# Performance work log

Measured on AMD Instinct MI355X. Metric: run time of the kernel, lower is better.

The kernel has to match this reference:

```python
import jax, jax.numpy as jnp
import numpy as np
from jax import lax

H = 512          # m_rnn_units
DIL = 2          # dilation
FH = 96          # forecast_horizon


def gru_step(x, h, Wih, Whh, bih, bhh):
    # torch.nn.GRU cell math
    gi = x @ Wih.T + bih          # [N, 3H]
    gh = h @ Whh.T + bhh          # [N, 3H]
    i_r, i_z, i_n = jnp.split(gi, 3, axis=-1)
    h_r, h_z, h_n = jnp.split(gh, 3, axis=-1)
    r = jax.nn.sigmoid(i_r + h_r)
    z = jax.nn.sigmoid(i_z + h_z)
    n = jnp.tanh(i_n + r * h_n)
    return (1.0 - z) * n + z * h


def setup_inputs() -> dict:
    key = jax.random.key(0)
    ks = jax.random.split(key, 10)
    s = 0.05
    return {
        "X0": jax.random.normal(ks[0], (64, 2 * H, 512), dtype=jnp.float32),
        "X1": jax.random.normal(ks[1], (64, H, FH), dtype=jnp.float32),
        "seqlen": 512,
        "W_ih_enc": jax.random.normal(ks[2], (3 * H, 2 * H), dtype=jnp.float32) * s,
        "W_hh_enc": jax.random.normal(ks[3], (3 * H, H), dtype=jnp.float32) * s,
        "b_ih_enc": jax.random.normal(ks[4], (3 * H,), dtype=jnp.float32) * s,
        "b_hh_enc": jax.random.normal(ks[5], (3 * H,), dtype=jnp.float32) * s,
        "W_ih_dec": jax.random.normal(ks[6], (3 * H, 2 * H), dtype=jnp.float32) * s,
        "W_hh_dec": jax.random.normal(ks[7], (3 * H, H), dtype=jnp.float32) * s,
        "b_ih_dec": jax.random.normal(ks[8], (3 * H,), dtype=jnp.float32) * s,
        "b_hh_dec": jax.random.normal(ks[9], (3 * H,), dtype=jnp.float32) * s,
    }


def reference(X0, X1, seqlen, W_ih_enc, W_hh_enc, b_ih_enc, b_hh_enc,
              W_ih_dec, W_hh_dec, b_ih_dec, b_hh_dec):
    B, C, T = X0.shape
    tgt_len = FH // DIL + 1
    N = B * DIL

    # ---- dilation reshuffle of history ----
    T2 = DIL * (T // DIL)
    X0c = X0[:, :, T - T2:]
    XX0 = jnp.stack([X0c[:, :, i::DIL] for i in range(DIL)])   # [d, B, C, T/d]
    XX0 = XX0.reshape(N, C, -1).transpose(0, 2, 1)             # [N, T/d, C]

    # ---- encoder GRU (scan over time) ----
    h0 = jnp.zeros((N, H), X0.dtype)

    def enc_step(h, xt):
        h2 = gru_step(xt, h, W_ih_enc, W_hh_enc, b_ih_enc, b_hh_enc)
        return h2, None

    h_enc, _ = lax.scan(enc_step, h0, XX0.transpose(1, 0, 2))  # [N, H]

    # ---- dilation reshuffle of covariates, pad to tgt_len*DIL ----
    pad = tgt_len * DIL - X1.shape[-1]
    X1p = jnp.pad(X1, ((0, 0), (0, 0), (0, pad)))
    XX1 = jnp.stack([X1p[:, :, i::DIL] for i in range(DIL)]).reshape(N, H, tgt_len)
    xs = XX1.transpose(2, 0, 1)                                # [tgt_len, N, H]

    def dec_step(carry, x1t):
        h, din = carry
        x = jnp.concatenate([din, x1t], axis=-1)               # [N, 2H]
        h2 = gru_step(x, h, W_ih_dec, W_hh_dec, b_ih_dec, b_hh_dec)
        return (h2, h2), h2

    _, outs = lax.scan(dec_step, (h_enc, h_enc), xs)           # [tgt_len, N, H]

    # ---- de-interleave back to original time order ----
    o = outs.transpose(1, 2, 0)                                # [N, H, tgt_len]
    o = o.reshape(DIL, B, H, tgt_len).transpose(1, 2, 3, 0)    # [B, H, tgt_len, d]
    o = o.reshape(B, H, tgt_len * DIL)
    return o[:, :, :FH]
```

## Files before the change

kernel.cpp:

```cpp
#include <hip/hip_runtime.h>


typedef __bf16 bf16x8 __attribute__((ext_vector_type(8)));
typedef float  f32x4  __attribute__((ext_vector_type(4)));
typedef unsigned int u32x4 __attribute__((ext_vector_type(4)));

#define MFMA16(a, b, c) __builtin_amdgcn_mfma_f32_16x16x32_bf16(a, b, c, 0, 0, 0)

#define OFF_FLG   0ULL
#define OFF_HB    16384ULL
#define OFF_XX0H  540672ULL
#define OFF_XX0L  67649536ULL
#define OFF_XX1H  134758400ULL
#define OFF_XX1L  141049856ULL
#define NEED_FULL 147341312ULL

static __device__ __forceinline__ void split_bf(float x, unsigned short& hi,
                                                unsigned short& lo) {
  union { __bf16 b; unsigned short u; } c;
  c.b = (__bf16)x; hi = c.u;
  float fh = (float)c.b;
  c.b = (__bf16)(x - fh); lo = c.u;
}
static __device__ __forceinline__ void split8(const float* __restrict__ p,
                                              bf16x8& h, bf16x8& l) {
#pragma unroll
  for (int j = 0; j < 8; ++j) {
    const float x = p[j];
    const __bf16 hb = (__bf16)x;
    h[j] = hb;
    l[j] = (__bf16)(x - (float)hb);
  }
}
static __device__ __forceinline__ void split8a(const float* xv, bf16x8& h, bf16x8& l) {
#pragma unroll
  for (int j = 0; j < 8; ++j) {
    const float x = xv[j];
    const __bf16 hb = (__bf16)x;
    h[j] = hb;
    l[j] = (__bf16)(x - (float)hb);
  }
}
static __device__ __forceinline__ float sigmoidf_(float x) {
  return 1.0f / (1.0f + __expf(-x));
}
static __device__ __forceinline__ float tanhf_(float x) {
  x = fminf(fmaxf(x, -15.0f), 15.0f);
  float e = __expf(2.0f * x);
  return (e - 1.0f) / (e + 1.0f);
}

static __device__ __forceinline__ void store_u32_mall(unsigned int* p,
                                                      unsigned int v) {
  asm volatile("global_store_dword %0, %1, off sc0 sc1"
               :: "v"(p), "v"(v) : "memory");
}
static __device__ __forceinline__ unsigned int load_u32_mall(const unsigned int* p) {
  unsigned int v;
  asm volatile("global_load_dword %0, %1, off sc0 sc1\n\t"
               "s_waitcnt vmcnt(0)"
               : "=v"(v) : "v"(p) : "memory");
  return v;
}
static __device__ __forceinline__ void load_h8_mall(const unsigned int* base,
                                                    u32x4 hv[4][2]) {
  asm volatile(
      "global_load_dwordx4 %0, %8, off sc0 sc1\n\t"
      "global_load_dwordx4 %1, %8, off offset:16 sc0 sc1\n\t"
      "global_load_dwordx4 %2, %8, off offset:128 sc0 sc1\n\t"
      "global_load_dwordx4 %3, %8, off offset:144 sc0 sc1\n\t"
      "global_load_dwordx4 %4, %8, off offset:256 sc0 sc1\n\t"
      "global_load_dwordx4 %5, %8, off offset:272 sc0 sc1\n\t"
      "global_load_dwordx4 %6, %8, off offset:384 sc0 sc1\n\t"
      "global_load_dwordx4 %7, %8, off offset:400 sc0 sc1\n\t"
      "s_waitcnt vmcnt(0)"
      : "=&v"(hv[0][0]), "=&v"(hv[0][1]), "=&v"(hv[1][0]), "=&v"(hv[1][1]),
        "=&v"(hv[2][0]), "=&v"(hv[2][1]), "=&v"(hv[3][0]), "=&v"(hv[3][1])
      : "v"(base)
      : "memory");
}

static __device__ __forceinline__ void wait_group(const unsigned int* __restrict__ flg,
                                                  int wave, int lane, unsigned int tgt) {
  if (wave == 0) {
    const unsigned int* fp = flg + (size_t)lane * 16;
    for (unsigned int it = 0; it < (1u << 20); ++it) {
      unsigned int v = tgt;
      if (lane < 32) v = load_u32_mall(fp);
      if (__all((int)(v >= tgt))) break;
      __builtin_amdgcn_s_sleep(1);
    }
  }
  __syncthreads();
}

static __device__ __forceinline__ void publish_group(unsigned int* myfl, int tid,
                                                     unsigned int val) {
  asm volatile("s_waitcnt vmcnt(0)" ::: "memory");
  __syncthreads();
  if (tid == 0) store_u32_mall(myfl, val);
}

__global__ void prep_x0(const float* __restrict__ X0, unsigned short* __restrict__ XH) {
  unsigned short* XL = XH + 33554432;
  __shared__ float tile[32][65];
  const int b  = blockIdx.x;
  const int c0 = blockIdx.y * 32;
  const int tid = threadIdx.x;
  for (int tb = 0; tb < 8; ++tb) {
    const int tau0 = tb * 64;
#pragma unroll
    for (int i = 0; i < 8; ++i) {
      const int cc  = (tid >> 6) + 4 * i;
      const int tau = tid & 63;
      tile[cc][tau] = X0[(size_t)b * 524288 + (size_t)(c0 + cc) * 512 + tau0 + tau];
    }
    __syncthreads();
#pragma unroll
    for (int s = 0; s < 8; ++s) {
      const int cc  = tid & 31;
      const int tau = (tid >> 5) * 8 + s;
      const int gt  = tau0 + tau;
      const int tt  = gt >> 1, d = gt & 1;
      unsigned short h, l;
      split_bf(tile[cc][tau], h, l);
      const size_t o = (size_t)tt * 131072 + (size_t)(d * 64 + b) * 1024 + c0 + cc;
      XH[o] = h; XL[o] = l;
    }
    __syncthreads();
  }
}

__global__ void prep_x1(const float* __restrict__ X1, unsigned short* __restrict__ XH) {
  unsigned short* XL = XH + 3145728;
  __shared__ float tile[32][97];
  const int b  = blockIdx.x;
  const int h0 = blockIdx.y * 32;
  const int tid = threadIdx.x;
#pragma unroll
  for (int i = 0; i < 12; ++i) {
    const int idx = i * 256 + tid;
    const int cc = idx / 96, tau = idx % 96;
    tile[cc][tau] = X1[(size_t)b * 49152 + (size_t)(h0 + cc) * 96 + tau];
  }
  __syncthreads();
#pragma unroll
  for (int i = 0; i < 12; ++i) {
    const int idx = i * 256 + tid;
    const int cc = idx & 31, tau = idx >> 5;
    const int tt = tau >> 1, d = tau & 1;
    unsigned short h, l;
    split_bf(tile[cc][tau], h, l);
    const size_t o = (size_t)tt * 65536 + (size_t)(d * 64 + b) * 512 + h0 + cc;
    XH[o] = h; XL[o] = l;
  }
}

template <bool STAGED>
__launch_bounds__(256, 1)
__global__ void rnn_persistent(unsigned char* __restrict__ ws,
                               const float* __restrict__ X0, const float* __restrict__ X1,
                               const float* __restrict__ WihE, const float* __restrict__ WhhE,
                               const float* __restrict__ bihE, const float* __restrict__ bhhE,
                               const float* __restrict__ WihD, const float* __restrict__ WhhD,
                               const float* __restrict__ bihD, const float* __restrict__ bhhD,
                               float* __restrict__ out) {
  const int tid  = threadIdx.x;
  const int wave = tid >> 6;
  const int lane = tid & 63;
  const int l15  = lane & 15;
  const int quad = lane >> 4;

  const int g  = blockIdx.x & 7;
  const int m  = blockIdx.x >> 3;
  const int rb = g * 16;
  const int ib = m * 16;

  const unsigned short* XX0H = (const unsigned short*)(ws + OFF_XX0H);
  const unsigned short* XX0L = (const unsigned short*)(ws + OFF_XX0L);
  const unsigned short* XX1H = (const unsigned short*)(ws + OFF_XX1H);
  const unsigned short* XX1L = (const unsigned short*)(ws + OFF_XX1L);
  unsigned int* HbP  = (unsigned int*)(ws + OFF_HB);
  unsigned int* flg  = (unsigned int*)(ws + OFF_FLG) + (size_t)g * 512;
  unsigned int* myfl = flg + (size_t)m * 16;

  __shared__ float red[4][6][256];

  const int r_row = tid >> 4;
  const int ii    = tid & 15;
  const int ig    = ib + ii;

  const int an    = rb + l15;
  const int ab    = an & 63, ad = an >> 6;
  const int onrow = rb + r_row;
  const int ob    = onrow & 63, od = onrow >> 6;

  const float bieR = bihE[ig], bieZ = bihE[512 + ig], bieN = bihE[1024 + ig];
  const float bheR = bhhE[ig], bheZ = bhhE[512 + ig], bheN = bhhE[1024 + ig];
  const float bidR = bihD[ig], bidZ = bihD[512 + ig], bidN = bihD[1024 + ig];
  const float bhdR = bhhD[ig], bhdZ = bhhD[512 + ig], bhdN = bhhD[1024 + ig];

  bf16x8 WIH_H[24], WIH_L[24], WHH_H[12], WHH_L[12];
#pragma unroll
  for (int kt = 0; kt < 8; ++kt)
#pragma unroll
    for (int nt = 0; nt < 3; ++nt)
      split8(WihE + (size_t)(nt * 512 + ib + l15) * 1024 + (wave * 8 + kt) * 32 + quad * 8,
             WIH_H[kt * 3 + nt], WIH_L[kt * 3 + nt]);
#pragma unroll
  for (int kt = 0; kt < 4; ++kt)
#pragma unroll
    for (int nt = 0; nt < 3; ++nt)
      split8(WhhE + (size_t)(nt * 512 + ib + l15) * 512 + (wave * 4 + kt) * 32 + quad * 8,
             WHH_H[kt * 3 + nt], WHH_L[kt * 3 + nt]);

  float h_reg = 0.0f;
  store_u32_mall(HbP + (size_t)onrow * 512 + ig, 0u);
  publish_group(myfl, tid, 1u);

  for (int t = 0; t < 256; ++t) {
    const int par  = t & 1;
    const int wpar = (t + 1) & 1;

    f32x4 gi0 = {0,0,0,0}, gi1 = {0,0,0,0}, gi2 = {0,0,0,0};
    const size_t xb  = ((size_t)t * 128 + an) * 1024 + quad * 8;
    const int    tau = 2 * t + ad;
#pragma unroll
    for (int kt = 0; kt < 8; ++kt) {
      bf16x8 axh, axl;
      if constexpr (STAGED) {
        axh = *reinterpret_cast<const bf16x8*>(XX0H + xb + (wave * 8 + kt) * 32);
        axl = *reinterpret_cast<const bf16x8*>(XX0L + xb + (wave * 8 + kt) * 32);
      } else {
        float xv[8];
#pragma unroll
        for (int j = 0; j < 8; ++j)
          xv[j] = X0[(size_t)ab * 524288 +
                     (size_t)((wave * 8 + kt) * 32 + quad * 8 + j) * 512 + tau];
        split8a(xv, axh, axl);
      }
      gi0 = MFMA16(axh, WIH_H[kt * 3 + 0], gi0);
      gi1 = MFMA16(axh, WIH_H[kt * 3 + 1], gi1);
      gi2 = MFMA16(axh, WIH_H[kt * 3 + 2], gi2);
      gi0 = MFMA16(axl, WIH_H[kt * 3 + 0], gi0);
      gi1 = MFMA16(axl, WIH_H[kt * 3 + 1], gi1);
      gi2 = MFMA16(axl, WIH_H[kt * 3 + 2], gi2);
      gi0 = MFMA16(axh, WIH_L[kt * 3 + 0], gi0);
      gi1 = MFMA16(axh, WIH_L[kt * 3 + 1], gi1);
      gi2 = MFMA16(axh, WIH_L[kt * 3 + 2], gi2);
    }

    wait_group(flg, wave, lane, (unsigned int)(t + 1));

    const unsigned int* hrow = HbP + (size_t)par * 65536 + (size_t)an * 512 + quad * 8;
    u32x4 hv[4][2];
    load_h8_mall(hrow + (size_t)wave * 128, hv);
    __builtin_amdgcn_sched_barrier(0);

    f32x4 gh0 = {0,0,0,0}, gh1 = {0,0,0,0}, gh2 = {0,0,0,0};
#pragma unroll
    for (int kt = 0; kt < 4; ++kt) {
      bf16x8 ahh, ahl;
      union { unsigned short u; __bf16 b; } c;
#pragma unroll
      for (int j = 0; j < 8; ++j) {
        const unsigned int w = hv[kt][j >> 2][j & 3];
        c.u = (unsigned short)(w & 0xffffu); ahh[j] = c.b;
        c.u = (unsigned short)(w >> 16);     ahl[j] = c.b;
      }
      gh0 = MFMA16(ahh, WHH_H[kt * 3 + 0], gh0);
      gh1 = MFMA16(ahh, WHH_H[kt * 3 + 1], gh1);
      gh2 = MFMA16(ahh, WHH_H[kt * 3 + 2], gh2);
      gh0 = MFMA16(ahl, WHH_H[kt * 3 + 0], gh0);
      gh1 = MFMA16(ahl, WHH_H[kt * 3 + 1], gh1);
      gh2 = MFMA16(ahl, WHH_H[kt * 3 + 2], gh2);
      gh0 = MFMA16(ahh, WHH_L[kt * 3 + 0], gh0);
      gh1 = MFMA16(ahh, WHH_L[kt * 3 + 1], gh1);
      gh2 = MFMA16(ahh, WHH_L[kt * 3 + 2], gh2);
    }

#pragma unroll
    for (int q = 0; q < 4; ++q) {
      const int base = (quad * 4 + q) * 16 + l15;
      red[wave][0][base] = gi0[q]; red[wave][1][base] = gi1[q]; red[wave][2][base] = gi2[q];
      red[wave][3][base] = gh0[q]; red[wave][4][base] = gh1[q]; red[wave][5][base] = gh2[q];
    }
    __syncthreads();
    float sR = 0, sZ = 0, sN = 0, hR = 0, hZ = 0, hN = 0;
#pragma unroll
    for (int w = 0; w < 4; ++w) {
      sR += red[w][0][tid]; sZ += red[w][1][tid]; sN += red[w][2][tid];
      hR += red[w][3][tid]; hZ += red[w][4][tid]; hN += red[w][5][tid];
    }
    const float rr = sigmoidf_(sR + bieR + hR + bheR);
    const float zz = sigmoidf_(sZ + bieZ + hZ + bheZ);
    const float nn = tanhf_(sN + bieN + rr * (hN + bheN));
    h_reg = (1.0f - zz) * nn + zz * h_reg;
    unsigned short ph, pl;
    split_bf(h_reg, ph, pl);
    store_u32_mall(HbP + (size_t)wpar * 65536 + (size_t)onrow * 512 + ig,
                   (unsigned int)ph | ((unsigned int)pl << 16));
    publish_group(myfl, tid, (unsigned int)(t + 2));
  }

  bf16x8 D1H[12], D1L[12], D2H[12], D2L[12], DHH[12], DHL[12];
#pragma unroll
  for (int kt = 0; kt < 4; ++kt)
#pragma unroll
    for (int nt = 0; nt < 3; ++nt) {
      const size_t row = (size_t)(nt * 512 + ib + l15);
      const int    k   = (wave * 4 + kt) * 32 + quad * 8;
      split8(WihD + row * 1024 + k,       D1H[kt * 3 + nt], D1L[kt * 3 + nt]);
      split8(WihD + row * 1024 + 512 + k, D2H[kt * 3 + nt], D2L[kt * 3 + nt]);
      split8(WhhD + row * 512 + k,        DHH[kt * 3 + nt], DHL[kt * 3 + nt]);
    }

  float* orow = out + (size_t)ob * 49152 + (size_t)ig * 96 + od;

  for (int t = 0; t < 48; ++t) {
    const int gt   = 256 + t;
    const int par  = gt & 1;
    const int wpar = (gt + 1) & 1;

    f32x4 gi0 = {0,0,0,0}, gi1 = {0,0,0,0}, gi2 = {0,0,0,0};
    const size_t x1b = ((size_t)t * 128 + an) * 512 + quad * 8;
    const int    tau = 2 * t + ad;
#pragma unroll
    for (int kt = 0; kt < 4; ++kt) {
      bf16x8 axh, axl;
      if constexpr (STAGED) {
        axh = *reinterpret_cast<const bf16x8*>(XX1H + x1b + (wave * 4 + kt) * 32);
        axl = *reinterpret_cast<const bf16x8*>(XX1L + x1b + (wave * 4 + kt) * 32);
      } else {
        float xv[8];
#pragma unroll
        for (int j = 0; j < 8; ++j)
          xv[j] = X1[(size_t)ab * 49152 +
                     (size_t)((wave * 4 + kt) * 32 + quad * 8 + j) * 96 + tau];
        split8a(xv, axh, axl);
      }
      gi0 = MFMA16(axh, D2H[kt * 3 + 0], gi0);
      gi1 = MFMA16(axh, D2H[kt * 3 + 1], gi1);
      gi2 = MFMA16(axh, D2H[kt * 3 + 2], gi2);
      gi0 = MFMA16(axl, D2H[kt * 3 + 0], gi0);
      gi1 = MFMA16(axl, D2H[kt * 3 + 1], gi1);
      gi2 = MFMA16(axl, D2H[kt * 3 + 2], gi2);
      gi0 = MFMA16(axh, D2L[kt * 3 + 0], gi0);
      gi1 = MFMA16(axh, D2L[kt * 3 + 1], gi1);
      gi2 = MFMA16(axh, D2L[kt * 3 + 2], gi2);
    }

    wait_group(flg, wave, lane, (unsigned int)(gt + 1));

    const unsigned int* hrow = HbP + (size_t)par * 65536 + (size_t)an * 512 + quad * 8;
    u32x4 hv[4][2];
    load_h8_mall(hrow + (size_t)wave * 128, hv);
    __builtin_amdgcn_sched_barrier(0);

    f32x4 gh0 = {0,0,0,0}, gh1 = {0,0,0,0}, gh2 = {0,0,0,0};
#pragma unroll
    for (int kt = 0; kt < 4; ++kt) {
      bf16x8 ahh, ahl;
      union { unsigned short u; __bf16 b; } c;
#pragma unroll
      for (int j = 0; j < 8; ++j) {
        const unsigned int w = hv[kt][j >> 2][j & 3];
        c.u = (unsigned short)(w & 0xffffu); ahh[j] = c.b;
        c.u = (unsigned short)(w >> 16);     ahl[j] = c.b;
      }
      gi0 = MFMA16(ahh, D1H[kt * 3 + 0], gi0);
      gi1 = MFMA16(ahh, D1H[kt * 3 + 1], gi1);
      gi2 = MFMA16(ahh, D1H[kt * 3 + 2], gi2);
      gi0 = MFMA16(ahl, D1H[kt * 3 + 0], gi0);
      gi1 = MFMA16(ahl, D1H[kt * 3 + 1], gi1);
      gi2 = MFMA16(ahl, D1H[kt * 3 + 2], gi2);
      gi0 = MFMA16(ahh, D1L[kt * 3 + 0], gi0);
      gi1 = MFMA16(ahh, D1L[kt * 3 + 1], gi1);
      gi2 = MFMA16(ahh, D1L[kt * 3 + 2], gi2);
      gh0 = MFMA16(ahh, DHH[kt * 3 + 0], gh0);
      gh1 = MFMA16(ahh, DHH[kt * 3 + 1], gh1);
      gh2 = MFMA16(ahh, DHH[kt * 3 + 2], gh2);
      gh0 = MFMA16(ahl, DHH[kt * 3 + 0], gh0);
      gh1 = MFMA16(ahl, DHH[kt * 3 + 1], gh1);
      gh2 = MFMA16(ahl, DHH[kt * 3 + 2], gh2);
      gh0 = MFMA16(ahh, DHL[kt * 3 + 0], gh0);
      gh1 = MFMA16(ahh, DHL[kt * 3 + 1], gh1);
      gh2 = MFMA16(ahh, DHL[kt * 3 + 2], gh2);
    }

#pragma unroll
    for (int q = 0; q < 4; ++q) {
      const int base = (quad * 4 + q) * 16 + l15;
      red[wave][0][base] = gi0[q]; red[wave][1][base] = gi1[q]; red[wave][2][base] = gi2[q];
      red[wave][3][base] = gh0[q]; red[wave][4][base] = gh1[q]; red[wave][5][base] = gh2[q];
    }
    __syncthreads();
    float sR = 0, sZ = 0, sN = 0, hR = 0, hZ = 0, hN = 0;
#pragma unroll
    for (int w = 0; w < 4; ++w) {
      sR += red[w][0][tid]; sZ += red[w][1][tid]; sN += red[w][2][tid];
      hR += red[w][3][tid]; hZ += red[w][4][tid]; hN += red[w][5][tid];
    }
    const float rr = sigmoidf_(sR + bidR + hR + bhdR);
    const float zz = sigmoidf_(sZ + bidZ + hZ + bhdZ);
    const float nn = tanhf_(sN + bidN + rr * (hN + bhdN));
    h_reg = (1.0f - zz) * nn + zz * h_reg;
    unsigned short ph, pl;
    split_bf(h_reg, ph, pl);
    store_u32_mall(HbP + (size_t)wpar * 65536 + (size_t)onrow * 512 + ig,
                   (unsigned int)ph | ((unsigned int)pl << 16));
    orow[2 * t] = h_reg;
    if (t < 47) {
      publish_group(myfl, tid, (unsigned int)(gt + 2));
    }
  }
}

extern "C" void kernel_launch(void* const* d_in, const int* in_sizes, int n_in,
                              void* d_out, int out_size, void* d_ws, size_t ws_size,
                              hipStream_t stream) {
  (void)in_sizes; (void)n_in; (void)out_size;
  const float* X0   = (const float*)d_in[0];
  const float* X1   = (const float*)d_in[1];
  const float* WihE = (const float*)d_in[3];
  const float* WhhE = (const float*)d_in[4];
  const float* bihE = (const float*)d_in[5];
  const float* bhhE = (const float*)d_in[6];
  const float* WihD = (const float*)d_in[7];
  const float* WhhD = (const float*)d_in[8];
  const float* bihD = (const float*)d_in[9];
  const float* bhhD = (const float*)d_in[10];
  unsigned char* ws = (unsigned char*)d_ws;

  const bool staged = (ws_size >= NEED_FULL);

  hipMemsetAsync(ws + OFF_FLG, 0, 16384, stream);
  if (staged) {
    prep_x0<<<dim3(64, 32), 256, 0, stream>>>(X0, (unsigned short*)(ws + OFF_XX0H));
    prep_x1<<<dim3(64, 16), 256, 0, stream>>>(X1, (unsigned short*)(ws + OFF_XX1H));
    rnn_persistent<true><<<256, 256, 0, stream>>>(ws, X0, X1, WihE, WhhE, bihE, bhhE,
                                                  WihD, WhhD, bihD, bhhD, (float*)d_out);
  } else {
    rnn_persistent<false><<<256, 256, 0, stream>>>(ws, X0, X1, WihE, WhhE, bihE, bhhE,
                                                   WihD, WhhD, bihD, bhhD, (float*)d_out);
  }
}
```

Baseline: 1.885 ms.

## Replace flag-based inter-block sync with parity-stamped hidden-state data polling

Removes the per-step flag publish and wait across the block group. Each stored hidden value now carries a parity stamp in the low bit of its low-bf16 half, and readers spin on the hidden-state loads until every stamp matches the expected step. This cuts a global flag round trip and a barrier chain from each recurrent step. In exchange it slightly perturbs the bf16 low-part precision and relies on word-level store visibility for correctness.

```diff
diff --git a/kernel.cpp b/kernel.cpp
--- a/kernel.cpp
+++ b/kernel.cpp
@@ -54,13 +54,6 @@
                                                       unsigned int v) {
   asm volatile("global_store_dword %0, %1, off sc0 sc1"
                :: "v"(p), "v"(v) : "memory");
-}
-static __device__ __forceinline__ unsigned int load_u32_mall(const unsigned int* p) {
-  unsigned int v;
-  asm volatile("global_load_dword %0, %1, off sc0 sc1\n\t"
-               "s_waitcnt vmcnt(0)"
-               : "=v"(v) : "v"(p) : "memory");
-  return v;
 }
 static __device__ __forceinline__ void load_h8_mall(const unsigned int* base,
                                                     u32x4 hv[4][2]) {
@@ -80,25 +73,22 @@
       : "memory");
 }
 
-static __device__ __forceinline__ void wait_group(const unsigned int* __restrict__ flg,
-                                                  int wave, int lane, unsigned int tgt) {
-  if (wave == 0) {
-    const unsigned int* fp = flg + (size_t)lane * 16;
-    for (unsigned int it = 0; it < (1u << 20); ++it) {
-      unsigned int v = tgt;
-      if (lane < 32) v = load_u32_mall(fp);
-      if (__all((int)(v >= tgt))) break;
-      __builtin_amdgcn_s_sleep(1);
-    }
-  }
-  __syncthreads();
-}
-
-static __device__ __forceinline__ void publish_group(unsigned int* myfl, int tid,
-                                                     unsigned int val) {
-  asm volatile("s_waitcnt vmcnt(0)" ::: "memory");
-  __syncthreads();
-  if (tid == 0) store_u32_mall(myfl, val);
+static __device__ __forceinline__ void load_h8_stamped(const unsigned int* base,
+                                                       u32x4 hv[4][2],
+                                                       unsigned int stamp) {
+  for (unsigned int it = 0; it < (1u << 20); ++it) {
+    load_h8_mall(base, hv);
+    unsigned int d = 0;
+#pragma unroll
+    for (int kt = 0; kt < 4; ++kt)
+#pragma unroll
+      for (int p = 0; p < 2; ++p)
+#pragma unroll
+        for (int j = 0; j < 4; ++j)
+          d |= ((hv[kt][p][j] >> 16) ^ stamp) & 1u;
+    if (__all((int)(d == 0))) break;
+  }
+  __builtin_amdgcn_sched_barrier(0);
 }
 
 __global__ void prep_x0(const float* __restrict__ X0, unsigned short* __restrict__ XH) {
@@ -181,8 +171,6 @@
   const unsigned short* XX1H = (const unsigned short*)(ws + OFF_XX1H);
   const unsigned short* XX1L = (const unsigned short*)(ws + OFF_XX1L);
   unsigned int* HbP  = (unsigned int*)(ws + OFF_HB);
-  unsigned int* flg  = (unsigned int*)(ws + OFF_FLG) + (size_t)g * 512;
-  unsigned int* myfl = flg + (size_t)m * 16;
 
   __shared__ float red[4][6][256];
 
@@ -215,12 +203,12 @@
              WHH_H[kt * 3 + nt], WHH_L[kt * 3 + nt]);
 
   float h_reg = 0.0f;
-  store_u32_mall(HbP + (size_t)onrow * 512 + ig, 0u);
-  publish_group(myfl, tid, 1u);
 
   for (int t = 0; t < 256; ++t) {
-    const int par  = t & 1;
-    const int wpar = (t + 1) & 1;
+    const int rslot = t & 1;
+    const int wslot = (t + 1) & 1;
+    const unsigned int rstamp = ((unsigned int)(t + 1) >> 1) & 1u;
+    const unsigned int wstamp = ((unsigned int)(t + 2) >> 1) & 1u;
 
     f32x4 gi0 = {0,0,0,0}, gi1 = {0,0,0,0}, gi2 = {0,0,0,0};
     const size_t xb  = ((size_t)t * 128 + an) * 1024 + quad * 8;
@@ -250,12 +238,9 @@
       gi2 = MFMA16(axh, WIH_L[kt * 3 + 2], gi2);
     }
 
-    wait_group(flg, wave, lane, (unsigned int)(t + 1));
-
-    const unsigned int* hrow = HbP + (size_t)par * 65536 + (size_t)an * 512 + quad * 8;
+    const unsigned int* hrow = HbP + (size_t)rslot * 65536 + (size_t)an * 512 + quad * 8;
     u32x4 hv[4][2];
-    load_h8_mall(hrow + (size_t)wave * 128, hv);
-    __builtin_amdgcn_sched_barrier(0);
+    load_h8_stamped(hrow + (size_t)wave * 128, hv, rstamp);
 
     f32x4 gh0 = {0,0,0,0}, gh1 = {0,0,0,0}, gh2 = {0,0,0,0};
 #pragma unroll
@@ -298,9 +283,9 @@
     h_reg = (1.0f - zz) * nn + zz * h_reg;
     unsigned short ph, pl;
     split_bf(h_reg, ph, pl);
-    store_u32_mall(HbP + (size_t)wpar * 65536 + (size_t)onrow * 512 + ig,
-                   (unsigned int)ph | ((unsigned int)pl << 16));
-    publish_group(myfl, tid, (unsigned int)(t + 2));
+    store_u32_mall(HbP + (size_t)wslot * 65536 + (size_t)onrow * 512 + ig,
+                   (unsigned int)ph | ((((unsigned int)pl & 0xFFFEu) | wstamp) << 16));
+    __syncthreads();
   }
 
   bf16x8 D1H[12], D1L[12], D2H[12], D2L[12], DHH[12], DHL[12];
@@ -318,9 +303,11 @@
   float* orow = out + (size_t)ob * 49152 + (size_t)ig * 96 + od;
 
   for (int t = 0; t < 48; ++t) {
-    const int gt   = 256 + t;
-    const int par  = gt & 1;
-    const int wpar = (gt + 1) & 1;
+    const int gt    = 256 + t;
+    const int rslot = gt & 1;
+    const int wslot = (gt + 1) & 1;
+    const unsigned int rstamp = ((unsigned int)(gt + 1) >> 1) & 1u;
+    const unsigned int wstamp = ((unsigned int)(gt + 2) >> 1) & 1u;
 
     f32x4 gi0 = {0,0,0,0}, gi1 = {0,0,0,0}, gi2 = {0,0,0,0};
     const size_t x1b = ((size_t)t * 128 + an) * 512 + quad * 8;
@@ -350,12 +337,9 @@
       gi2 = MFMA16(axh, D2L[kt * 3 + 2], gi2);
     }
 
-    wait_group(flg, wave, lane, (unsigned int)(gt + 1));
-
-    const unsigned int* hrow = HbP + (size_t)par * 65536 + (size_t)an * 512 + quad * 8;
+    const unsigned int* hrow = HbP + (size_t)rslot * 65536 + (size_t)an * 512 + quad * 8;
     u32x4 hv[4][2];
-    load_h8_mall(hrow + (size_t)wave * 128, hv);
-    __builtin_amdgcn_sched_barrier(0);
+    load_h8_stamped(hrow + (size_t)wave * 128, hv, rstamp);
 
     f32x4 gh0 = {0,0,0,0}, gh1 = {0,0,0,0}, gh2 = {0,0,0,0};
 #pragma unroll
@@ -407,12 +391,10 @@
     h_reg = (1.0f - zz) * nn + zz * h_reg;
     unsigned short ph, pl;
     split_bf(h_reg, ph, pl);
-    store_u32_mall(HbP + (size_t)wpar * 65536 + (size_t)onrow * 512 + ig,
-                   (unsigned int)ph | ((unsigned int)pl << 16));
+    store_u32_mall(HbP + (size_t)wslot * 65536 + (size_t)onrow * 512 + ig,
+                   (unsigned int)ph | ((((unsigned int)pl & 0xFFFEu) | wstamp) << 16));
     orow[2 * t] = h_reg;
-    if (t < 47) {
-      publish_group(myfl, tid, (unsigned int)(gt + 2));
-    }
+    __syncthreads();
   }
 }
 
@@ -434,7 +416,7 @@
 
   const bool staged = (ws_size >= NEED_FULL);
 
-  hipMemsetAsync(ws + OFF_FLG, 0, 16384, stream);
+  hipMemsetAsync(ws + OFF_HB, 0, 524288, stream);
   if (staged) {
     prep_x0<<<dim3(64, 32), 256, 0, stream>>>(X0, (unsigned short*)(ws + OFF_XX0H));
     prep_x1<<<dim3(64, 16), 256, 0, stream>>>(X1, (unsigned short*)(ws + OFF_XX1H));
```

After: 1.697 ms. 1.11x faster.
